# Optimization experiments

Hardware: AMD Instinct MI355X
Metric: run time of the kernel (lower is better)

Reference implementation:

```python
import jax, jax.numpy as jnp
import numpy as np

E = 1024  # embedding_size
H = 16    # num_heads
D = E // H  # head_size = 64
SCALE = 1.0 / np.sqrt(np.float32(E))  # NOTE: original scales by sqrt(embedding_size), not head_size


def setup_inputs() -> dict:
    key = jax.random.key(0)
    ks = jax.random.split(key, 11)
    B, S = 2, 2048
    init = 1.0 / np.sqrt(np.float32(E))
    inp = {
        'q': jax.random.normal(ks[0], (B, S, E), dtype=jnp.float32),
        'k': jax.random.normal(ks[1], (B, S, E), dtype=jnp.float32),
        'v': jax.random.normal(ks[2], (B, S, E), dtype=jnp.float32),
        'wq': jax.random.normal(ks[3], (E, E), dtype=jnp.float32) * init,
        'bq': jax.random.normal(ks[4], (E,), dtype=jnp.float32) * init,
        'wk': jax.random.normal(ks[5], (E, E), dtype=jnp.float32) * init,
        'bk': jax.random.normal(ks[6], (E,), dtype=jnp.float32) * init,
        'wv': jax.random.normal(ks[7], (E, E), dtype=jnp.float32) * init,
        'bv': jax.random.normal(ks[8], (E,), dtype=jnp.float32) * init,
        'wo': jax.random.normal(ks[9], (E, E), dtype=jnp.float32) * init,
        'bo': jax.random.normal(ks[10], (E,), dtype=jnp.float32) * init,
    }
    return inp


def reference(q, k, v, wq, bq, wk, bk, wv, bv, wo, bo):
    S = q.shape[1]
    # Linear projections (torch Linear: x @ W.T + b)
    qp = (q @ wq.T + bq).reshape(-1, H, S, D)  # faithful raw view, not transpose
    kp = (k @ wk.T + bk).reshape(-1, H, S, D)
    vp = (v @ wv.T + bv).reshape(-1, H, S, D)
    # scores / sqrt(embedding_size) -- faithful to original (uses E, not D)
    scores = jnp.einsum('bhqd,bhkd->bhqk', qp, kp) * SCALE
    attn = jax.nn.softmax(scores, axis=-1)  # [B,H,S,S]
    out = jnp.einsum('bhqk,bhkd->bhqd', attn, vp)  # [B,H,S,D]
    out = out.reshape(-1, S, E)
    # dropout is eval-mode identity
    return out @ wo.T + bo
```

## Files before the change

kernel.cpp:

```cpp
#include <hip/hip_runtime.h>
#include <hip/hip_bf16.h>
#include <cstdint>


typedef __bf16 bf16_t;
typedef bf16_t bf16x8 __attribute__((ext_vector_type(8)));
typedef bf16_t bf16x4 __attribute__((ext_vector_type(4)));
typedef float  f32x4  __attribute__((ext_vector_type(4)));
typedef float  f32x16 __attribute__((ext_vector_type(16)));
typedef unsigned int u32;
typedef u32 u32x2 __attribute__((ext_vector_type(2)));

#define MFMA16(a, b, c) __builtin_amdgcn_mfma_f32_16x16x32_bf16((a), (b), (c), 0, 0, 0)
#define MFMA32(a, b, c) __builtin_amdgcn_mfma_f32_32x32x16_bf16((a), (b), (c), 0, 0, 0)

#define GLOAD_LDS16(gptr, lptr)                                                      \
  __builtin_amdgcn_global_load_lds(                                                  \
      (const __attribute__((address_space(1))) void*)(gptr),                         \
      (__attribute__((address_space(3))) void*)(lptr), 16, 0, 0)

namespace {
constexpr int kS = 2048, kE = 1024, kD = 64;
constexpr int kM = 4096;
constexpr float kQScaleL2E = 0.03125f * 1.44269504088896f;
}

__device__ inline u32 pkbf(float a, float b) {
  u32 r;
  asm("v_cvt_pk_bf16_f32 %0, %1, %2" : "=v"(r) : "v"(a), "v"(b));
  return r;
}

__device__ inline bf16x8 make_pfrag(float v0, float v1, float v2, float v3,
                                    float v4, float v5, float v6, float v7) {
  u32 A0 = pkbf(v0, v1), A1 = pkbf(v2, v3);
  u32 B0 = pkbf(v4, v5), B1 = pkbf(v6, v7);
  u32x2 r0 = __builtin_amdgcn_permlane32_swap(A0, B0, false, false);
  u32x2 r1 = __builtin_amdgcn_permlane32_swap(A1, B1, false, false);
  union { u32 w[4]; bf16x8 v; } u;
  u.w[0] = r0[0]; u.w[1] = r1[0]; u.w[2] = r0[1]; u.w[3] = r1[1];
  return u.v;
}

__device__ inline float xhalf_sum(float x) {
  u32 xu = __builtin_bit_cast(u32, x);
  u32x2 r = __builtin_amdgcn_permlane32_swap(xu, xu, false, false);
  return __builtin_bit_cast(float, r[0]) + __builtin_bit_cast(float, r[1]);
}

__global__ void cvt_batch(const float* __restrict__ s0, const float* __restrict__ s1,
                          const float* __restrict__ s2, const float* __restrict__ s3,
                          bf16_t* __restrict__ d0, bf16_t* __restrict__ d1,
                          bf16_t* __restrict__ d2, bf16_t* __restrict__ d3, int n4) {
  const float* s; bf16_t* d;
  switch (blockIdx.y) {
    case 0:  s = s0; d = d0; break;
    case 1:  s = s1; d = d1; break;
    case 2:  s = s2; d = d2; break;
    default: s = s3; d = d3; break;
  }
  int stride = gridDim.x * blockDim.x;
  for (int i = blockIdx.x * blockDim.x + threadIdx.x; i < n4; i += stride) {
    float4 v = reinterpret_cast<const float4*>(s)[i];
    bf16x4 o;
    o[0] = (bf16_t)v.x; o[1] = (bf16_t)v.y; o[2] = (bf16_t)v.z; o[3] = (bf16_t)v.w;
    reinterpret_cast<bf16x4*>(d)[i] = o;
  }
}

__global__ __launch_bounds__(256, 3)
void gemm_qkv(const bf16_t* __restrict__ qb, const bf16_t* __restrict__ kb,
              const bf16_t* __restrict__ vb, const bf16_t* __restrict__ W,
              const float* __restrict__ bq, const float* __restrict__ bk,
              const float* __restrict__ bv,
              bf16_t* __restrict__ Qp, bf16_t* __restrict__ Kp, bf16_t* __restrict__ Vp) {
  constexpr int K = kE, BK = 64;
  __shared__ __align__(16) bf16_t As[128 * BK];
  __shared__ __align__(16) bf16_t Bs[128 * BK];
  const int tid = threadIdx.x, lane = tid & 63, wave = tid >> 6;
  const int fr = lane & 15, fg = lane >> 4;
  const int region = blockIdx.x >> 3;
  const int bm = blockIdx.y * 128, bn = blockIdx.x * 128;
  const int bnl = (blockIdx.x & 7) * 128;
  const bf16_t* A = region == 0 ? qb : region == 1 ? kb : vb;
  const float* bias = region == 0 ? bq : region == 1 ? bk : bv;
  bf16_t* Cp = region == 0 ? Qp : region == 1 ? Kp : Vp;
  const float scale = region == 0 ? kQScaleL2E : 1.0f;
  const int wr = (wave >> 1) * 64, wc = (wave & 1) * 64;
  f32x4 acc[4][4] = {};
  for (int k0 = 0; k0 < K; k0 += BK) {
#pragma unroll
    for (int c = 0; c < 4; ++c) {
      int lin = c * 256 + tid, row = lin >> 3, ch = lin & 7, sch = ch ^ (row & 7);
      GLOAD_LDS16(A + (size_t)(bm + row) * K + k0 + sch * 8, (char*)As + lin * 16);
    }
#pragma unroll
    for (int c = 0; c < 4; ++c) {
      int lin = c * 256 + tid, row = lin >> 3, ch = lin & 7, sch = ch ^ (row & 7);
      GLOAD_LDS16(W + (size_t)(bn + row) * K + k0 + sch * 8, (char*)Bs + lin * 16);
    }
    __syncthreads();
#pragma unroll
    for (int kk = 0; kk < 2; ++kk) {
      bf16x8 af[4], bfv[4];
#pragma unroll
      for (int i = 0; i < 4; ++i) {
        int row = wr + i * 16 + fr;
        int ch = (kk * 4 + fg) ^ (row & 7);
        af[i] = *reinterpret_cast<const bf16x8*>((const char*)As + row * 128 + ch * 16);
      }
#pragma unroll
      for (int j = 0; j < 4; ++j) {
        int row = wc + j * 16 + fr;
        int ch = (kk * 4 + fg) ^ (row & 7);
        bfv[j] = *reinterpret_cast<const bf16x8*>((const char*)Bs + row * 128 + ch * 16);
      }
#pragma unroll
      for (int i = 0; i < 4; ++i)
#pragma unroll
        for (int j = 0; j < 4; ++j)
          acc[i][j] = MFMA16(af[i], bfv[j], acc[i][j]);
    }
    __syncthreads();
  }
#pragma unroll
  for (int i = 0; i < 4; ++i)
#pragma unroll
    for (int j = 0; j < 4; ++j) {
      int coll = bnl + wc + j * 16 + fr;
      float bvv = bias[coll];
#pragma unroll
      for (int r = 0; r < 4; ++r) {
        int row = bm + wr + i * 16 + fg * 4 + r;
        Cp[(size_t)row * kE + coll] = (bf16_t)((acc[i][j][r] + bvv) * scale);
      }
    }
}

__global__ __launch_bounds__(256, 3)
void gemm_out(const bf16_t* __restrict__ A, const bf16_t* __restrict__ Bm,
              const float* __restrict__ bias, float* __restrict__ Cout) {
  constexpr int K = kE, BK = 64;
  __shared__ __align__(16) bf16_t As[128 * BK];
  __shared__ __align__(16) bf16_t Bs[64 * BK];
  const int tid = threadIdx.x, lane = tid & 63, wave = tid >> 6;
  const int fr = lane & 15, fg = lane >> 4;
  const int bm = blockIdx.y * 128, bn = blockIdx.x * 64;
  const int wr = wave * 32;
  f32x4 acc[2][4] = {};
  for (int k0 = 0; k0 < K; k0 += BK) {
#pragma unroll
    for (int c = 0; c < 4; ++c) {
      int lin = c * 256 + tid, row = lin >> 3, ch = lin & 7, sch = ch ^ (row & 7);
      GLOAD_LDS16(A + (size_t)(bm + row) * K + k0 + sch * 8, (char*)As + lin * 16);
    }
#pragma unroll
    for (int c = 0; c < 2; ++c) {
      int lin = c * 256 + tid, row = lin >> 3, ch = lin & 7, sch = ch ^ (row & 7);
      GLOAD_LDS16(Bm + (size_t)(bn + row) * K + k0 + sch * 8, (char*)Bs + lin * 16);
    }
    __syncthreads();
#pragma unroll
    for (int kk = 0; kk < 2; ++kk) {
      bf16x8 af[2], bfv[4];
#pragma unroll
      for (int i = 0; i < 2; ++i) {
        int row = wr + i * 16 + fr;
        int ch = (kk * 4 + fg) ^ (row & 7);
        af[i] = *reinterpret_cast<const bf16x8*>((const char*)As + row * 128 + ch * 16);
      }
#pragma unroll
      for (int j = 0; j < 4; ++j) {
        int row = j * 16 + fr;
        int ch = (kk * 4 + fg) ^ (row & 7);
        bfv[j] = *reinterpret_cast<const bf16x8*>((const char*)Bs + row * 128 + ch * 16);
      }
#pragma unroll
      for (int i = 0; i < 2; ++i)
#pragma unroll
        for (int j = 0; j < 4; ++j)
          acc[i][j] = MFMA16(af[i], bfv[j], acc[i][j]);
    }
    __syncthreads();
  }
#pragma unroll
  for (int i = 0; i < 2; ++i)
#pragma unroll
    for (int j = 0; j < 4; ++j) {
      int col = bn + j * 16 + fr;
      float bvv = bias[col];
#pragma unroll
      for (int r = 0; r < 4; ++r) {
        int row = bm + wr + i * 16 + fg * 4 + r;
        Cout[(size_t)row * kE + col] = acc[i][j][r] + bvv;
      }
    }
}

__global__ __launch_bounds__(256)
void vtranspose(const bf16_t* __restrict__ Vp, bf16_t* __restrict__ VpT) {
  __shared__ __align__(16) bf16_t T[256 * 64];
  const int tid = threadIdx.x;
  const size_t hb = (size_t)blockIdx.y * (kS * kD);
  const bf16_t* src = Vp + hb + (size_t)blockIdx.x * 256 * kD;
  bf16_t* dst = VpT + hb + blockIdx.x * 256;
#pragma unroll
  for (int c = 0; c < 8; ++c) {
    int lin = c * 256 + tid;
    int row = lin >> 3, ch = lin & 7;
    bf16x8 v = *reinterpret_cast<const bf16x8*>(src + row * kD + ch * 8);
    *reinterpret_cast<bf16x8*>((char*)T + row * 128 + ((ch ^ ((row >> 3) & 7)) * 16)) = v;
  }
  __syncthreads();
#pragma unroll
  for (int c = 0; c < 8; ++c) {
    int lin = c * 256 + tid;
    int d = lin >> 5, kc = lin & 31;
    bf16x8 o;
#pragma unroll
    for (int e = 0; e < 8; ++e) {
      int s = kc * 8 + e;
      o[e] = *reinterpret_cast<const bf16_t*>(
          (const char*)T + s * 128 + (((d >> 3) ^ ((s >> 3) & 7)) * 16) + (d & 7) * 2);
    }
    *reinterpret_cast<bf16x8*>(dst + (size_t)d * kS + kc * 8) = o;
  }
}

__global__ __launch_bounds__(512, 4)
void attn_fwd(const bf16_t* __restrict__ Qp, const bf16_t* __restrict__ Kp,
              const bf16_t* __restrict__ VpT, bf16_t* __restrict__ Op) {
  __shared__ __align__(16) char smem[66048];
  const int tid = threadIdx.x, lane = tid & 63, wave = tid >> 6;
  const int ql = lane & 31, hi = lane >> 5;
  const int g = wave >> 2, ws = wave & 3;
  const int tg = tid & 255;
  const int newb = ((int)blockIdx.x & 7) * 64 + ((int)blockIdx.x >> 3);
  const int head = newb >> 4, qt = newb & 15;
  const size_t hbase = (size_t)head * (kS * kD);
  const int q0 = qt * 128 + ws * 32;
  char* const gbase = smem + g * 32768;
  const bf16_t* Kh = Kp + hbase + (size_t)(g * 1024) * kD;
  const bf16_t* Vh = VpT + hbase + g * 1024;

  bf16x8 qf[4];
#pragma unroll
  for (int ct = 0; ct < 4; ++ct)
    qf[ct] = *reinterpret_cast<const bf16x8*>(
        Qp + hbase + (size_t)(q0 + ql) * kD + ct * 16 + hi * 8);

  float Lp = 0.0f;
  f32x16 o0 = {}, o1 = {};

  auto STAGE = [&](int kt) {
    const bf16_t* Kt = Kh + (size_t)kt * 64 * kD;
    const bf16_t* Vt = Vh + kt * 64;
    char* Kd = gbase + (kt & 1) * 16384;
    char* Vd = Kd + 8192;
#pragma unroll
    for (int c = 0; c < 2; ++c) {
      int lin = c * 256 + tg, row = lin >> 3, ch = lin & 7, sch = ch ^ (row & 7);
      GLOAD_LDS16(Kt + row * kD + sch * 8, Kd + lin * 16);
    }
#pragma unroll
    for (int c = 0; c < 2; ++c) {
      int lin = c * 256 + tg, row = lin >> 3, ch = lin & 7, sch = ch ^ (row & 7);
      GLOAD_LDS16(Vt + (size_t)row * kS + sch * 8, Vd + lin * 16);
    }
  };

  STAGE(0);
#pragma unroll 1
  for (int kt = 0; kt < 16; ++kt) {
    __syncthreads();
    const char* Kb = gbase + (kt & 1) * 16384;
    const char* Vb = Kb + 8192;
    if (kt + 1 < 16) STAGE(kt + 1);

    f32x16 s0 = {}, s1 = {};
    __builtin_amdgcn_s_setprio(1);
#pragma unroll
    for (int ct = 0; ct < 4; ++ct) {
      bf16x8 k0 = *reinterpret_cast<const bf16x8*>(
          Kb + ql * 128 + (((2 * ct + hi) ^ (ql & 7)) * 16));
      bf16x8 k1 = *reinterpret_cast<const bf16x8*>(
          Kb + (32 + ql) * 128 + (((2 * ct + hi) ^ (ql & 7)) * 16));
      s0 = MFMA32(k0, qf[ct], s0);
      s1 = MFMA32(k1, qf[ct], s1);
    }
    __builtin_amdgcn_s_setprio(0);

    float a0 = 0.f, a1 = 0.f;
#pragma unroll
    for (int r = 0; r < 16; ++r) {
      s0[r] = __builtin_amdgcn_exp2f(s0[r]);
      s1[r] = __builtin_amdgcn_exp2f(s1[r]);
      a0 += s0[r]; a1 += s1[r];
    }
    Lp += a0 + a1;

    bf16x8 pf0 = make_pfrag(s0[0], s0[1], s0[2], s0[3], s0[4], s0[5], s0[6], s0[7]);
    bf16x8 pf1 = make_pfrag(s0[8], s0[9], s0[10], s0[11], s0[12], s0[13], s0[14], s0[15]);
    bf16x8 pf2 = make_pfrag(s1[0], s1[1], s1[2], s1[3], s1[4], s1[5], s1[6], s1[7]);
    bf16x8 pf3 = make_pfrag(s1[8], s1[9], s1[10], s1[11], s1[12], s1[13], s1[14], s1[15]);

    __builtin_amdgcn_s_setprio(1);
#pragma unroll
    for (int j = 0; j < 4; ++j) {
      bf16x8 v0 = *reinterpret_cast<const bf16x8*>(
          Vb + ql * 128 + (((2 * j + hi) ^ (ql & 7)) * 16));
      bf16x8 v1 = *reinterpret_cast<const bf16x8*>(
          Vb + (32 + ql) * 128 + (((2 * j + hi) ^ (ql & 7)) * 16));
      bf16x8 pj = (j == 0) ? pf0 : (j == 1) ? pf1 : (j == 2) ? pf2 : pf3;
      o0 = MFMA32(v0, pj, o0);
      o1 = MFMA32(v1, pj, o1);
    }
    __builtin_amdgcn_s_setprio(0);
  }

  __syncthreads();
  if (g == 1) {
    char* pb = smem + 32768 + ws * 8192;
#pragma unroll
    for (int c = 0; c < 4; ++c) {
      *reinterpret_cast<f32x4*>(pb + c * 1024 + lane * 16) =
          (f32x4){o0[4 * c], o0[4 * c + 1], o0[4 * c + 2], o0[4 * c + 3]};
      *reinterpret_cast<f32x4*>(pb + 4096 + c * 1024 + lane * 16) =
          (f32x4){o1[4 * c], o1[4 * c + 1], o1[4 * c + 2], o1[4 * c + 3]};
    }
    float Lb = xhalf_sum(Lp);
    if (hi == 0) *reinterpret_cast<float*>(smem + 65536 + (ws * 32 + ql) * 4) = Lb;
  }
  __syncthreads();
  if (g == 0) {
    const char* pb = smem + 32768 + ws * 8192;
#pragma unroll
    for (int c = 0; c < 4; ++c) {
      f32x4 r0 = *reinterpret_cast<const f32x4*>(pb + c * 1024 + lane * 16);
      f32x4 r1 = *reinterpret_cast<const f32x4*>(pb + 4096 + c * 1024 + lane * 16);
#pragma unroll
      for (int i = 0; i < 4; ++i) { o0[4 * c + i] += r0[i]; o1[4 * c + i] += r1[i]; }
    }
    float L = xhalf_sum(Lp) +
              *reinterpret_cast<const float*>(smem + 65536 + (ws * 32 + ql) * 4);
    float inv = 1.0f / L;
#pragma unroll
    for (int r = 0; r < 16; ++r) { o0[r] *= inv; o1[r] *= inv; }
    const int wb = ws * 4096;
#pragma unroll
    for (int c = 0; c < 4; ++c) {
      {
        u32 w0 = pkbf(o0[4 * c + 0], o0[4 * c + 1]);
        u32 w1 = pkbf(o0[4 * c + 2], o0[4 * c + 3]);
        int d0 = 8 * c + 4 * hi;
        int byte = (wb + ql * 128 + d0 * 2) ^ ((ql & 7) << 4);
        *reinterpret_cast<u32x2*>(smem + byte) = (u32x2){w0, w1};
      }
      {
        u32 w0 = pkbf(o1[4 * c + 0], o1[4 * c + 1]);
        u32 w1 = pkbf(o1[4 * c + 2], o1[4 * c + 3]);
        int d0 = 32 + 8 * c + 4 * hi;
        int byte = (wb + ql * 128 + d0 * 2) ^ ((ql & 7) << 4);
        *reinterpret_cast<u32x2*>(smem + byte) = (u32x2){w0, w1};
      }
    }
    asm volatile("s_waitcnt lgkmcnt(0)" ::: "memory");
    __builtin_amdgcn_sched_barrier(0);
#pragma unroll
    for (int it = 0; it < 4; ++it) {
      int lin = it * 64 + lane;
      int qr = lin >> 3, ch = lin & 7;
      int byte = wb + qr * 128 + ((ch * 16) ^ ((qr & 7) << 4));
      bf16x8 vrow = *reinterpret_cast<const bf16x8*>(smem + byte);
      *reinterpret_cast<bf16x8*>(Op + hbase + (size_t)(q0 + qr) * kD + ch * 8) = vrow;
    }
  }
}

extern "C" void kernel_launch(void* const* d_in, const int* in_sizes, int n_in,
                              void* d_out, int out_size, void* d_ws, size_t ws_size,
                              hipStream_t stream) {
  (void)in_sizes; (void)n_in; (void)out_size; (void)ws_size;
  const float* q  = (const float*)d_in[0];
  const float* k  = (const float*)d_in[1];
  const float* v  = (const float*)d_in[2];
  const float* wq = (const float*)d_in[3];
  const float* bq = (const float*)d_in[4];
  const float* wk = (const float*)d_in[5];
  const float* bk = (const float*)d_in[6];
  const float* wv = (const float*)d_in[7];
  const float* bv = (const float*)d_in[8];
  const float* wo = (const float*)d_in[9];
  const float* bo = (const float*)d_in[10];
  float* out = (float*)d_out;

  char* ws = (char*)d_ws;
  const size_t MB = 1ull << 20;
  bf16_t* qb   = (bf16_t*)(ws +  0 * MB);
  bf16_t* kb   = (bf16_t*)(ws +  8 * MB);
  bf16_t* vb   = (bf16_t*)(ws + 16 * MB);
  bf16_t* wqkv = (bf16_t*)(ws + 24 * MB);
  bf16_t* wob  = (bf16_t*)(ws + 30 * MB);
  bf16_t* Qp   = (bf16_t*)(ws + 32 * MB);
  bf16_t* Kp   = (bf16_t*)(ws + 40 * MB);
  bf16_t* Vp   = (bf16_t*)(ws + 48 * MB);
  bf16_t* Opb  = (bf16_t*)(ws + 56 * MB);
  bf16_t* VpT  = (bf16_t*)(ws +  0 * MB);

  const int nQKV4 = (kM * kE) / 4;
  const int nW4 = (kE * kE) / 4;
  cvt_batch<<<dim3(512, 3), 256, 0, stream>>>(q, k, v, v, qb, kb, vb, vb, nQKV4);
  cvt_batch<<<dim3(128, 4), 256, 0, stream>>>(wq, wk, wv, wo, wqkv, wqkv + 1048576,
                                              wqkv + 2097152, wob, nW4);

  gemm_qkv<<<dim3(24, 32), 256, 0, stream>>>(qb, kb, vb, wqkv, bq, bk, bv, Qp, Kp, Vp);

  vtranspose<<<dim3(kS / 256, 32), 256, 0, stream>>>(Vp, VpT);

  attn_fwd<<<dim3(512), 512, 0, stream>>>(Qp, Kp, VpT, Opb);

  gemm_out<<<dim3(16, 32), 256, 0, stream>>>(Opb, wob, bo, out);
}
```

Baseline: 120.6 us.

## Process 64 query rows per wave to reuse K/V fragments across two Q tiles

Each wave in the attention kernel now handles two 32-row query tiles, so every K and V fragment read from LDS feeds two MFMAs instead of one. The block covers 256 queries, the grid is halved to 256 blocks, and the launch bound drops to 2 blocks per CU to leave room for the doubled accumulators. The epilogue reduction buffer moves to the start of shared memory and writes both tiles. This reduces LDS traffic and K/V staging per query, at the cost of higher register pressure, fewer blocks in flight and possibly less occupancy across the CUs.

```diff
diff --git a/kernel.cpp b/kernel.cpp
--- a/kernel.cpp
+++ b/kernel.cpp
@@ -227,30 +227,33 @@
   }
 }
 
-__global__ __launch_bounds__(512, 4)
+__global__ __launch_bounds__(512, 2)
 void attn_fwd(const bf16_t* __restrict__ Qp, const bf16_t* __restrict__ Kp,
               const bf16_t* __restrict__ VpT, bf16_t* __restrict__ Op) {
-  __shared__ __align__(16) char smem[66048];
+  __shared__ __align__(16) char smem[66560];
   const int tid = threadIdx.x, lane = tid & 63, wave = tid >> 6;
   const int ql = lane & 31, hi = lane >> 5;
   const int g = wave >> 2, ws = wave & 3;
   const int tg = tid & 255;
-  const int newb = ((int)blockIdx.x & 7) * 64 + ((int)blockIdx.x >> 3);
-  const int head = newb >> 4, qt = newb & 15;
+  const int newb = ((int)blockIdx.x & 7) * 32 + ((int)blockIdx.x >> 3);
+  const int head = newb >> 3, qt = newb & 7;
   const size_t hbase = (size_t)head * (kS * kD);
-  const int q0 = qt * 128 + ws * 32;
+  const int q0 = qt * 256 + ws * 64;
   char* const gbase = smem + g * 32768;
   const bf16_t* Kh = Kp + hbase + (size_t)(g * 1024) * kD;
   const bf16_t* Vh = VpT + hbase + g * 1024;
 
-  bf16x8 qf[4];
-#pragma unroll
-  for (int ct = 0; ct < 4; ++ct)
-    qf[ct] = *reinterpret_cast<const bf16x8*>(
+  bf16x8 qfA[4], qfB[4];
+#pragma unroll
+  for (int ct = 0; ct < 4; ++ct) {
+    qfA[ct] = *reinterpret_cast<const bf16x8*>(
         Qp + hbase + (size_t)(q0 + ql) * kD + ct * 16 + hi * 8);
-
-  float Lp = 0.0f;
-  f32x16 o0 = {}, o1 = {};
+    qfB[ct] = *reinterpret_cast<const bf16x8*>(
+        Qp + hbase + (size_t)(q0 + 32 + ql) * kD + ct * 16 + hi * 8);
+  }
+
+  float LpA = 0.0f, LpB = 0.0f;
+  f32x16 oA0 = {}, oA1 = {}, oB0 = {}, oB1 = {};
 
   auto STAGE = [&](int kt) {
     const bf16_t* Kt = Kh + (size_t)kt * 64 * kD;
@@ -277,7 +280,7 @@
     const char* Vb = Kb + 8192;
     if (kt + 1 < 16) STAGE(kt + 1);
 
-    f32x16 s0 = {}, s1 = {};
+    f32x16 sA0 = {}, sA1 = {}, sB0 = {}, sB1 = {};
     __builtin_amdgcn_s_setprio(1);
 #pragma unroll
     for (int ct = 0; ct < 4; ++ct) {
@@ -285,24 +288,33 @@
           Kb + ql * 128 + (((2 * ct + hi) ^ (ql & 7)) * 16));
       bf16x8 k1 = *reinterpret_cast<const bf16x8*>(
           Kb + (32 + ql) * 128 + (((2 * ct + hi) ^ (ql & 7)) * 16));
-      s0 = MFMA32(k0, qf[ct], s0);
-      s1 = MFMA32(k1, qf[ct], s1);
+      sA0 = MFMA32(k0, qfA[ct], sA0);
+      sA1 = MFMA32(k1, qfA[ct], sA1);
+      sB0 = MFMA32(k0, qfB[ct], sB0);
+      sB1 = MFMA32(k1, qfB[ct], sB1);
     }
     __builtin_amdgcn_s_setprio(0);
 
-    float a0 = 0.f, a1 = 0.f;
+    float aA = 0.f, aB = 0.f;
 #pragma unroll
     for (int r = 0; r < 16; ++r) {
-      s0[r] = __builtin_amdgcn_exp2f(s0[r]);
-      s1[r] = __builtin_amdgcn_exp2f(s1[r]);
-      a0 += s0[r]; a1 += s1[r];
-    }
-    Lp += a0 + a1;
-
-    bf16x8 pf0 = make_pfrag(s0[0], s0[1], s0[2], s0[3], s0[4], s0[5], s0[6], s0[7]);
-    bf16x8 pf1 = make_pfrag(s0[8], s0[9], s0[10], s0[11], s0[12], s0[13], s0[14], s0[15]);
-    bf16x8 pf2 = make_pfrag(s1[0], s1[1], s1[2], s1[3], s1[4], s1[5], s1[6], s1[7]);
-    bf16x8 pf3 = make_pfrag(s1[8], s1[9], s1[10], s1[11], s1[12], s1[13], s1[14], s1[15]);
+      sA0[r] = __builtin_amdgcn_exp2f(sA0[r]);
+      sA1[r] = __builtin_amdgcn_exp2f(sA1[r]);
+      sB0[r] = __builtin_amdgcn_exp2f(sB0[r]);
+      sB1[r] = __builtin_amdgcn_exp2f(sB1[r]);
+      aA += sA0[r] + sA1[r];
+      aB += sB0[r] + sB1[r];
+    }
+    LpA += aA; LpB += aB;
+
+    bf16x8 pA0 = make_pfrag(sA0[0], sA0[1], sA0[2], sA0[3], sA0[4], sA0[5], sA0[6], sA0[7]);
+    bf16x8 pA1 = make_pfrag(sA0[8], sA0[9], sA0[10], sA0[11], sA0[12], sA0[13], sA0[14], sA0[15]);
+    bf16x8 pA2 = make_pfrag(sA1[0], sA1[1], sA1[2], sA1[3], sA1[4], sA1[5], sA1[6], sA1[7]);
+    bf16x8 pA3 = make_pfrag(sA1[8], sA1[9], sA1[10], sA1[11], sA1[12], sA1[13], sA1[14], sA1[15]);
+    bf16x8 pB0 = make_pfrag(sB0[0], sB0[1], sB0[2], sB0[3], sB0[4], sB0[5], sB0[6], sB0[7]);
+    bf16x8 pB1 = make_pfrag(sB0[8], sB0[9], sB0[10], sB0[11], sB0[12], sB0[13], sB0[14], sB0[15]);
+    bf16x8 pB2 = make_pfrag(sB1[0], sB1[1], sB1[2], sB1[3], sB1[4], sB1[5], sB1[6], sB1[7]);
+    bf16x8 pB3 = make_pfrag(sB1[8], sB1[9], sB1[10], sB1[11], sB1[12], sB1[13], sB1[14], sB1[15]);
 
     __builtin_amdgcn_s_setprio(1);
 #pragma unroll
@@ -311,68 +323,97 @@
           Vb + ql * 128 + (((2 * j + hi) ^ (ql & 7)) * 16));
       bf16x8 v1 = *reinterpret_cast<const bf16x8*>(
           Vb + (32 + ql) * 128 + (((2 * j + hi) ^ (ql & 7)) * 16));
-      bf16x8 pj = (j == 0) ? pf0 : (j == 1) ? pf1 : (j == 2) ? pf2 : pf3;
-      o0 = MFMA32(v0, pj, o0);
-      o1 = MFMA32(v1, pj, o1);
+      bf16x8 pA = (j == 0) ? pA0 : (j == 1) ? pA1 : (j == 2) ? pA2 : pA3;
+      bf16x8 pB = (j == 0) ? pB0 : (j == 1) ? pB1 : (j == 2) ? pB2 : pB3;
+      oA0 = MFMA32(v0, pA, oA0);
+      oA1 = MFMA32(v1, pA, oA1);
+      oB0 = MFMA32(v0, pB, oB0);
+      oB1 = MFMA32(v1, pB, oB1);
     }
     __builtin_amdgcn_s_setprio(0);
   }
 
   __syncthreads();
   if (g == 1) {
-    char* pb = smem + 32768 + ws * 8192;
+    char* pb = smem + ws * 16384;
 #pragma unroll
     for (int c = 0; c < 4; ++c) {
       *reinterpret_cast<f32x4*>(pb + c * 1024 + lane * 16) =
-          (f32x4){o0[4 * c], o0[4 * c + 1], o0[4 * c + 2], o0[4 * c + 3]};
+          (f32x4){oA0[4 * c], oA0[4 * c + 1], oA0[4 * c + 2], oA0[4 * c + 3]};
       *reinterpret_cast<f32x4*>(pb + 4096 + c * 1024 + lane * 16) =
-          (f32x4){o1[4 * c], o1[4 * c + 1], o1[4 * c + 2], o1[4 * c + 3]};
-    }
-    float Lb = xhalf_sum(Lp);
-    if (hi == 0) *reinterpret_cast<float*>(smem + 65536 + (ws * 32 + ql) * 4) = Lb;
+          (f32x4){oA1[4 * c], oA1[4 * c + 1], oA1[4 * c + 2], oA1[4 * c + 3]};
+      *reinterpret_cast<f32x4*>(pb + 8192 + c * 1024 + lane * 16) =
+          (f32x4){oB0[4 * c], oB0[4 * c + 1], oB0[4 * c + 2], oB0[4 * c + 3]};
+      *reinterpret_cast<f32x4*>(pb + 12288 + c * 1024 + lane * 16) =
+          (f32x4){oB1[4 * c], oB1[4 * c + 1], oB1[4 * c + 2], oB1[4 * c + 3]};
+    }
+    float LA = xhalf_sum(LpA), LB = xhalf_sum(LpB);
+    if (hi == 0) {
+      *reinterpret_cast<float*>(smem + 65536 + (ws * 64 + ql) * 4) = LA;
+      *reinterpret_cast<float*>(smem + 65536 + (ws * 64 + 32 + ql) * 4) = LB;
+    }
   }
   __syncthreads();
   if (g == 0) {
-    const char* pb = smem + 32768 + ws * 8192;
+    const char* pb = smem + ws * 16384;
 #pragma unroll
     for (int c = 0; c < 4; ++c) {
-      f32x4 r0 = *reinterpret_cast<const f32x4*>(pb + c * 1024 + lane * 16);
-      f32x4 r1 = *reinterpret_cast<const f32x4*>(pb + 4096 + c * 1024 + lane * 16);
-#pragma unroll
-      for (int i = 0; i < 4; ++i) { o0[4 * c + i] += r0[i]; o1[4 * c + i] += r1[i]; }
-    }
-    float L = xhalf_sum(Lp) +
-              *reinterpret_cast<const float*>(smem + 65536 + (ws * 32 + ql) * 4);
-    float inv = 1.0f / L;
-#pragma unroll
-    for (int r = 0; r < 16; ++r) { o0[r] *= inv; o1[r] *= inv; }
-    const int wb = ws * 4096;
-#pragma unroll
-    for (int c = 0; c < 4; ++c) {
-      {
-        u32 w0 = pkbf(o0[4 * c + 0], o0[4 * c + 1]);
-        u32 w1 = pkbf(o0[4 * c + 2], o0[4 * c + 3]);
-        int d0 = 8 * c + 4 * hi;
-        int byte = (wb + ql * 128 + d0 * 2) ^ ((ql & 7) << 4);
-        *reinterpret_cast<u32x2*>(smem + byte) = (u32x2){w0, w1};
-      }
-      {
-        u32 w0 = pkbf(o1[4 * c + 0], o1[4 * c + 1]);
-        u32 w1 = pkbf(o1[4 * c + 2], o1[4 * c + 3]);
-        int d0 = 32 + 8 * c + 4 * hi;
-        int byte = (wb + ql * 128 + d0 * 2) ^ ((ql & 7) << 4);
-        *reinterpret_cast<u32x2*>(smem + byte) = (u32x2){w0, w1};
-      }
-    }
-    asm volatile("s_waitcnt lgkmcnt(0)" ::: "memory");
-    __builtin_amdgcn_sched_barrier(0);
-#pragma unroll
-    for (int it = 0; it < 4; ++it) {
-      int lin = it * 64 + lane;
-      int qr = lin >> 3, ch = lin & 7;
-      int byte = wb + qr * 128 + ((ch * 16) ^ ((qr & 7) << 4));
-      bf16x8 vrow = *reinterpret_cast<const bf16x8*>(smem + byte);
-      *reinterpret_cast<bf16x8*>(Op + hbase + (size_t)(q0 + qr) * kD + ch * 8) = vrow;
+      f32x4 rA0 = *reinterpret_cast<const f32x4*>(pb + c * 1024 + lane * 16);
+      f32x4 rA1 = *reinterpret_cast<const f32x4*>(pb + 4096 + c * 1024 + lane * 16);
+      f32x4 rB0 = *reinterpret_cast<const f32x4*>(pb + 8192 + c * 1024 + lane * 16);
+      f32x4 rB1 = *reinterpret_cast<const f32x4*>(pb + 12288 + c * 1024 + lane * 16);
+#pragma unroll
+      for (int i = 0; i < 4; ++i) {
+        oA0[4 * c + i] += rA0[i]; oA1[4 * c + i] += rA1[i];
+        oB0[4 * c + i] += rB0[i]; oB1[4 * c + i] += rB1[i];
+      }
+    }
+    float LA = xhalf_sum(LpA) +
+               *reinterpret_cast<const float*>(smem + 65536 + (ws * 64 + ql) * 4);
+    float LB = xhalf_sum(LpB) +
+               *reinterpret_cast<const float*>(smem + 65536 + (ws * 64 + 32 + ql) * 4);
+    float invA = 1.0f / LA, invB = 1.0f / LB;
+#pragma unroll
+    for (int r = 0; r < 16; ++r) {
+      oA0[r] *= invA; oA1[r] *= invA; oB0[r] *= invB; oB1[r] *= invB;
+    }
+#pragma unroll
+    for (int X = 0; X < 2; ++X) {
+      const int wb = ws * 16384 + X * 4096;
+      const int qX = q0 + X * 32;
+#pragma unroll
+      for (int c = 0; c < 4; ++c) {
+        float e00 = X ? oB0[4 * c + 0] : oA0[4 * c + 0];
+        float e01 = X ? oB0[4 * c + 1] : oA0[4 * c + 1];
+        float e02 = X ? oB0[4 * c + 2] : oA0[4 * c + 2];
+        float e03 = X ? oB0[4 * c + 3] : oA0[4 * c + 3];
+        float e10 = X ? oB1[4 * c + 0] : oA1[4 * c + 0];
+        float e11 = X ? oB1[4 * c + 1] : oA1[4 * c + 1];
+        float e12 = X ? oB1[4 * c + 2] : oA1[4 * c + 2];
+        float e13 = X ? oB1[4 * c + 3] : oA1[4 * c + 3];
+        {
+          u32 w0 = pkbf(e00, e01), w1 = pkbf(e02, e03);
+          int d0 = 8 * c + 4 * hi;
+          int byte = (wb + ql * 128 + d0 * 2) ^ ((ql & 7) << 4);
+          *reinterpret_cast<u32x2*>(smem + byte) = (u32x2){w0, w1};
+        }
+        {
+          u32 w0 = pkbf(e10, e11), w1 = pkbf(e12, e13);
+          int d0 = 32 + 8 * c + 4 * hi;
+          int byte = (wb + ql * 128 + d0 * 2) ^ ((ql & 7) << 4);
+          *reinterpret_cast<u32x2*>(smem + byte) = (u32x2){w0, w1};
+        }
+      }
+      asm volatile("s_waitcnt lgkmcnt(0)" ::: "memory");
+      __builtin_amdgcn_sched_barrier(0);
+#pragma unroll
+      for (int it = 0; it < 4; ++it) {
+        int lin = it * 64 + lane;
+        int qr = lin >> 3, ch = lin & 7;
+        int byte = wb + qr * 128 + ((ch * 16) ^ ((qr & 7) << 4));
+        bf16x8 vrow = *reinterpret_cast<const bf16x8*>(smem + byte);
+        *reinterpret_cast<bf16x8*>(Op + hbase + (size_t)(qX + qr) * kD + ch * 8) = vrow;
+      }
     }
   }
 }
@@ -417,7 +458,7 @@
 
   vtranspose<<<dim3(kS / 256, 32), 256, 0, stream>>>(Vp, VpT);
 
-  attn_fwd<<<dim3(512), 512, 0, stream>>>(Qp, Kp, VpT, Opb);
+  attn_fwd<<<dim3(256), 512, 0, stream>>>(Qp, Kp, VpT, Opb);
 
   gemm_out<<<dim3(16, 32), 256, 0, stream>>>(Opb, wob, bo, out);
 }
```

Result: faster. 117.4 us (-2.7%).
